# Kernel tuning notes

Measured on AMD Instinct MI355X. Metric: run time of the kernel, lower is better.

## Reference

```python
import jax, jax.numpy as jnp
import numpy as np

NUM_CLASSES = 4
TRAIN_SWITCH = True
TOPO = {1: {0: 1, 1: 0}, 2: {0: 1, 1: 1}, 3: {0: 2, 1: 0}, 4: {0: 1, 1: 0}}


def _sublevel_h0(v, H, W, eight):
    """0-dim sublevel-set persistence of a 2D grid via union-find.

    v: flat numpy array of length H*W. eight: 8-connectivity (gudhi
    T-construction, lower cells = min of cofaces) vs 4-connectivity (dual).
    Returns (pairs, essential_idx): pairs is a list of (birth_idx, death_idx)
    pixel indices with strictly positive persistence; essential_idx is the
    pixel index of the global-min (essential, death = +inf) component.
    """
    N = H * W
    order = np.argsort(v, kind='stable')
    rank = np.empty(N, np.int64)
    rank[order] = np.arange(N)
    parent = np.full(N, -1, np.int64)   # -1 = not yet in filtration
    creator = np.zeros(N, np.int64)     # pixel realizing the component's birth
    pairs = []

    def find(a):
        root = a
        while parent[root] != root:
            root = parent[root]
        while parent[a] != root:
            parent[a], a = root, parent[a]
        return root

    offs = [(-1, 0), (1, 0), (0, -1), (0, 1)]
    if eight:
        offs += [(-1, -1), (-1, 1), (1, -1), (1, 1)]
    for idx in order:
        idx = int(idx)
        r, c = divmod(idx, W)
        parent[idx] = idx
        creator[idx] = idx
        for dr, dc in offs:
            rr, cc = r + dr, c + dc
            if 0 <= rr < H and 0 <= cc < W:
                nb = rr * W + cc
                if parent[nb] >= 0:
                    ra, rb = find(idx), find(nb)
                    if ra != rb:
                        # elder rule: component with earlier (smaller) birth survives
                        if rank[creator[ra]] < rank[creator[rb]]:
                            elder, young = ra, rb
                        else:
                            elder, young = rb, ra
                        if v[idx] > v[creator[young]]:  # drop 0-persistence pairs (gudhi default)
                            pairs.append((int(creator[young]), idx))
                        parent[young] = elder
    ess = int(creator[find(int(order[0]))])
    return pairs, ess


def _diagrams(img):
    """H0 and H1 persistence pairs (as pixel indices) of a 2D image,
    matching gudhi.CubicalComplex(top_dimensional_cells=img).persistence().
    H0: sublevel union-find with 8-connectivity. H1 by Alexander duality:
    superlevel H0 with 4-connectivity, pairs reversed."""
    H, W = img.shape
    v = img.ravel()
    h0, ess = _sublevel_h0(v, H, W, eight=True)
    sup, _ = _sublevel_h0(-v, H, W, eight=False)
    h1 = [(d, b) for (b, d) in sup]  # (saddle birth, max death)
    pers = lambda p: v[p[1]] - v[p[0]]
    h0.sort(key=pers, reverse=True)  # gudhi orders by decreasing persistence
    h1.sort(key=pers, reverse=True)
    return h0, ess, h1


def _dim_loss(flat, pairs, ess_idx, nf):
    """loss_per_dimension: first nf pairs are 'kept' -> (1-pers)^2, missing
    features cost 1 each, extra pairs cost pers^2. Essential (death=inf)
    pair has pers = 1 - birth and sorts first (infinite persistence)."""
    parts = []
    if ess_idx is not None:
        parts.append((1.0 - flat[ess_idx])[None])
    if pairs:
        b = np.asarray([p[0] for p in pairs], np.int64)
        d = np.asarray([p[1] for p in pairs], np.int64)
        parts.append(flat[d] - flat[b])
    pvec = jnp.concatenate(parts) if parts else jnp.zeros((0,), flat.dtype)
    n = pvec.shape[0]
    return jnp.sum((1.0 - pvec[:nf]) ** 2) + float(max(0, nf - n)) + jnp.sum(pvec[nf:] ** 2)


def setup_inputs() -> dict:
    key = jax.random.key(0)
    # (1, batch, classes, H, W); values in [0,1] like softmax probabilities
    x = jax.random.uniform(key, (1, 4, NUM_CLASSES, 64, 64), dtype=jnp.float32)
    return {"x": x}


def reference(x):
    xs = x[0]  # squeeze(0) -> (B, C, H, W)
    if not TRAIN_SWITCH:
        xs = jnp.clip(1.0 - xs, 0.0, 1.0)
    xn = np.asarray(xs)
    B, C, H, W = xn.shape
    loss = jnp.zeros((), jnp.float32)
    for b in range(B):
        for c in range(1, C):  # skip background class 0
            h0, ess, h1 = _diagrams(xn[b, c])
            flat = xs[b, c].ravel()
            loss = loss + _dim_loss(flat, h0, ess, TOPO[c][0])
            loss = loss + _dim_loss(flat, h1, None, TOPO[c][1])
    return loss / B
```

## Files before the change

kernel.cpp:

```cpp
#include <hip/hip_runtime.h>

#define NPIX 4096
#define NT 1024
#define PPT (NPIX / NT)
#define EMPTY 0xFFFFFFFFu
#define FLAGMAGIC 0x00C0FFEEu

__global__ void ph_zero_kernel(float* out) { out[0] = 0.0f; }

__device__ __forceinline__ float kval(unsigned k) {
  unsigned u = (k & 0x80000000u) ? (k & 0x7FFFFFFFu) : ~k;
  return __uint_as_float(u);
}

__global__ __launch_bounds__(NT) void ph_pass_kernel(const float* __restrict__ x,
                                                     float* __restrict__ out,
                                                     unsigned long long* __restrict__ ws64,
                                                     int use_ws) {
  __shared__ unsigned long long pool[2 * NPIX];
  __shared__ unsigned long long claim64[NPIX];
  __shared__ unsigned long long wred[32];
  __shared__ int s_chg[13];
  __shared__ double s_sum[16];
  __shared__ float s_max[16];
  __shared__ int s_cnt[16];

  unsigned long long* sbuf = pool;
  unsigned* hkey = (unsigned*)pool;
  unsigned* hval = hkey + NPIX;
  unsigned* key32 = (unsigned*)(pool + NPIX);
  unsigned short* label = (unsigned short*)(pool + NPIX + NPIX / 2);
  unsigned long long* node = pool + NPIX;

  const int blk = blockIdx.x;
  const int b = blk / 6;
  const int rem = blk % 6;
  const int c = (rem >> 1) + 1;
  const int pass = rem & 1;
  const float* img = x + (size_t)(b * 4 + c) * NPIX;
  const int tid = threadIdx.x;
  const int lane = tid & 63, wid = tid >> 6;
  const int ndirs = pass ? 4 : 8;
  const int drr[8] = {-1, 1, 0, 0, -1, -1, 1, 1};
  const int dcc[8] = { 0, 0,-1, 1, -1,  1, -1, 1};

  if (tid < 13) s_chg[tid] = 0;
  unsigned lmin = EMPTY;
  for (int i = tid; i < NPIX; i += NT) {
    float f = img[i];
    if (pass) f = -f;
    unsigned u = __float_as_uint(f);
    unsigned k = (u & 0x80000000u) ? ~u : (u | 0x80000000u);
    key32[i] = k;
    pool[i] = ~0ull;
    claim64[i] = 0ull;
    lmin = min(lmin, k);
  }
  for (int off = 32; off > 0; off >>= 1)
    lmin = min(lmin, (unsigned)__shfl_xor((int)lmin, off));
  if (lane == 0) wred[wid] = lmin;
  __syncthreads();
  unsigned vmink = (unsigned)wred[0];
  #pragma unroll
  for (int w = 1; w < 16; w++) vmink = min(vmink, (unsigned)wred[w]);

  for (int i = tid; i < NPIX; i += NT) {
    unsigned long long best = ((unsigned long long)key32[i] << 32) | (unsigned)i;
    int bestnb = i;
    int r = i >> 6, cc = i & 63;
    for (int d = 0; d < ndirs; d++) {
      int rr = r + drr[d], c2 = cc + dcc[d];
      if ((unsigned)rr >= 64u || (unsigned)c2 >= 64u) continue;
      int nb = (rr << 6) | c2;
      unsigned long long pn = ((unsigned long long)key32[nb] << 32) | (unsigned)nb;
      if (pn < best) { best = pn; bestnb = nb; }
    }
    label[i] = (unsigned short)bestnb;
  }
  __syncthreads();
  for (int round = 0; round < 6; round++) {
    bool changed = false;
    for (int i = tid; i < NPIX; i += NT) {
      unsigned short l = label[i];
      unsigned short l2 = label[l];
      unsigned short l3 = label[l2];
      unsigned short l4 = label[l3];
      if (l4 != l) { label[i] = l4; changed = true; }
    }
    if (changed) s_chg[round] = 1;
    __syncthreads();
    if (!s_chg[round]) break;
  }

  const int pdr[4] = {1, 0, 1,  1};
  const int pdc[4] = {0, 1, 1, -1};
  const int npd = pass ? 2 : 4;
  for (int i = tid; i < NPIX; i += NT) {
    int r = i >> 6, cc = i & 63;
    unsigned la = label[i];
    unsigned ki = key32[i];
    for (int d = 0; d < npd; d++) {
      int rr = r + pdr[d], c2 = cc + pdc[d];
      if ((unsigned)rr >= 64u || (unsigned)c2 >= 64u) continue;
      int nb = (rr << 6) | c2;
      unsigned lb = label[nb];
      if (lb == la) continue;
      unsigned wkey = max(ki, key32[nb]);
      unsigned pk = la < lb ? ((la << 12) | lb) : ((lb << 12) | la);
      unsigned h = (pk * 2654435761u) >> 20;
      while (true) {
        unsigned old = atomicCAS(&hkey[h], EMPTY, pk);
        if (old == EMPTY || old == pk) { atomicMin(&hval[h], wkey); break; }
        h = (h + 1) & (NPIX - 1);
      }
    }
  }
  __syncthreads();

  unsigned long long item[PPT];
  unsigned mykeys[PPT];
  int cnt = 0;
  #pragma unroll
  for (int q = 0; q < PPT; q++) {
    int s = tid * PPT + q;
    unsigned pk = hkey[s];
    if (pk != EMPTY) item[cnt++] = (((unsigned long long)hval[s]) << 32) | pk;
  }
  #pragma unroll
  for (int t = 0; t < PPT; t++) mykeys[t] = key32[tid + t * NT];
  __syncthreads();
  unsigned inc = (unsigned)cnt;
  for (int off = 1; off < 64; off <<= 1) {
    unsigned v = __shfl_up(inc, off);
    if (lane >= off) inc += v;
  }
  if (lane == 63) wred[wid] = inc;
  __syncthreads();
  if (wid == 0) {
    unsigned wv = (lane < 16) ? (unsigned)wred[lane] : 0u;
    for (int off = 1; off < 16; off <<= 1) {
      unsigned v = __shfl_up(wv, off);
      if (lane >= off) wv += v;
    }
    if (lane < 16) wred[16 + lane] = wv;
  }
  __syncthreads();
  const int M = (int)wred[31];
  const int base0 = (int)((wid ? (unsigned)wred[16 + wid - 1] : 0u) + inc) - cnt;
  for (int q = 0; q < cnt; q++) sbuf[base0 + q] = item[q];
  #pragma unroll
  for (int t = 0; t < PPT; t++) {
    int i = tid + t * NT;
    node[i] = (((unsigned long long)mykeys[t]) << 32) | (unsigned)i;
  }
  if (tid < 2) s_chg[tid] = 0;
  __syncthreads();

  double sumsq = 0.0;
  float maxp = 0.0f;
  int pcnt = 0;
  unsigned ewk[PPT], exa[PPT], exb[PPT];
  unsigned long long erA[PPT], erB[PPT];
  unsigned pmask = 0;
  #pragma unroll
  for (int q = 0; q < PPT; q++) {
    const int j = tid + q * NT;
    if (j < M) {
      const unsigned long long e = sbuf[j];
      ewk[q] = (unsigned)(e >> 32);
      const unsigned pk = (unsigned)(e & 0xFFFFFFu);
      unsigned xa = pk >> 12, xb = pk & 0xFFFu;
      exa[q] = xa; exb[q] = xb;
      erA[q] = node[xa]; erB[q] = node[xb];
      pmask |= 1u << q;
    }
  }
  unsigned long long seqtag = (1ull << 44);
  #pragma unroll
  for (int q = 0; q < PPT; q++) {
    if (pmask & (1u << q)) {
      const int j = tid + q * NT;
      const unsigned long long myval =
          seqtag | (((unsigned long long)(~ewk[q])) << 12) | (unsigned)j;
      unsigned young, elder;
      if (erA[q] < erB[q]) { elder = exa[q]; young = exb[q]; }
      else                 { elder = exb[q]; young = exa[q]; }
      if (claim64[young] < myval) atomicMax(&claim64[young], myval);
      if (claim64[elder] < myval) atomicMax(&claim64[elder], myval);
    }
  }
  int rt = 1;
  while (true) {
    __syncthreads();
    #pragma unroll
    for (int q = 0; q < PPT; q++) {
      if (pmask & (1u << q)) {
        const int j = tid + q * NT;
        const unsigned long long myval =
            seqtag | (((unsigned long long)(~ewk[q])) << 12) | (unsigned)j;
        unsigned young, elder;
        unsigned long long yrec;
        if (erA[q] < erB[q]) { elder = exa[q]; young = exb[q]; yrec = erB[q]; }
        else                 { elder = exb[q]; young = exa[q]; yrec = erA[q]; }
        if (claim64[young] == myval) {
          const unsigned ky = (unsigned)(yrec >> 32);
          if (ewk[q] > ky) {
            float pers = kval(ewk[q]) - kval(ky);
            sumsq += (double)pers * (double)pers;
            maxp = fmaxf(maxp, pers);
            pcnt++;
          }
          node[young] = (yrec & 0xFFFFFFFF00000000ull) | elder;
          pmask &= ~(1u << q);
        }
      }
    }
    if (pmask) s_chg[rt & 1] = 1;
    if (tid == 0) s_chg[(rt + 1) & 1] = 0;
    __syncthreads();
    if (!s_chg[rt & 1]) break;
    rt++; seqtag += (1ull << 44);
    #pragma unroll
    for (int q = 0; q < PPT; q++) {
      if (pmask & (1u << q)) {
        unsigned xa = exa[q], xb = exb[q];
        unsigned long long recA = node[xa], recB = node[xb];
        while ((unsigned)recA != xa) { xa = (unsigned)recA; recA = node[xa]; }
        while ((unsigned)recB != xb) { xb = (unsigned)recB; recB = node[xb]; }
        exa[q] = xa; exb[q] = xb; erA[q] = recA; erB[q] = recB;
        if (xa == xb) {
          pmask &= ~(1u << q);
        } else {
          const int j = tid + q * NT;
          const unsigned long long myval =
              seqtag | (((unsigned long long)(~ewk[q])) << 12) | (unsigned)j;
          unsigned young, elder;
          if (recA < recB) { elder = xa; young = xb; }
          else             { elder = xb; young = xa; }
          if (claim64[young] < myval) atomicMax(&claim64[young], myval);
          if (claim64[elder] < myval) atomicMax(&claim64[elder], myval);
        }
      }
    }
  }
  for (int off = 32; off > 0; off >>= 1) {
    sumsq += __shfl_xor(sumsq, off);
    maxp = fmaxf(maxp, __shfl_xor(maxp, off));
    pcnt += __shfl_xor(pcnt, off);
  }
  if (lane == 0) { s_sum[wid] = sumsq; s_max[wid] = maxp; s_cnt[wid] = pcnt; }
  __syncthreads();

  float contrib = 0.0f;
  if (tid == 0) {
    #pragma unroll
    for (int w = 1; w < 16; w++) {
      sumsq += s_sum[w];
      maxp = fmaxf(maxp, s_max[w]);
      pcnt += s_cnt[w];
    }
    if (pass == 0) {
      const int nf0 = (c == 3) ? 2 : 1;
      float vmin = kval(vmink);
      if (nf0 == 1) {
        contrib = vmin * vmin + (float)sumsq;
      } else if (pcnt >= 1) {
        contrib = vmin * vmin + (1.0f - maxp) * (1.0f - maxp)
                + (float)(sumsq - (double)maxp * (double)maxp);
      } else {
        contrib = vmin * vmin + 1.0f;
      }
    } else {
      const int nf1 = (c == 2) ? 1 : 0;
      if (nf1 == 0) contrib = (float)sumsq;
      else contrib = (pcnt >= 1)
        ? ((1.0f - maxp) * (1.0f - maxp) + (float)(sumsq - (double)maxp * (double)maxp))
        : 1.0f;
    }
    contrib *= 0.25f;
    if (use_ws) {
      atomicExch(&ws64[blk],
                 (((unsigned long long)__float_as_uint(contrib)) << 32) | FLAGMAGIC);
    } else {
      atomicAdd(out, contrib);
    }
  }
  if (use_ws && blk == 0 && wid == 0) {
    float v = 0.0f;
    if (lane < 24) {
      while (true) {
        unsigned long long r = atomicAdd(&ws64[lane], 0ull);
        if ((unsigned)r == FLAGMAGIC) { v = __uint_as_float((unsigned)(r >> 32)); break; }
      }
    }
    for (int off = 32; off > 0; off >>= 1) v += __shfl_xor(v, off);
    if (lane == 0) out[0] = v;
  }
}

extern "C" void kernel_launch(void* const* d_in, const int* in_sizes, int n_in,
                              void* d_out, int out_size, void* d_ws, size_t ws_size,
                              hipStream_t stream) {
  const float* x = (const float*)d_in[0];
  float* out = (float*)d_out;
  if (ws_size >= 24 * sizeof(unsigned long long)) {
    ph_pass_kernel<<<24, NT, 0, stream>>>(x, out, (unsigned long long*)d_ws, 1);
  } else {
    ph_zero_kernel<<<1, 1, 0, stream>>>(out);
    ph_pass_kernel<<<24, NT, 0, stream>>>(x, out, nullptr, 0);
  }
}
```

Baseline: 94.32 us.

## Hand off the union-find merge tail to a single wavefront when few edges remain

The iterative claim/resolve merge rounds now count the remaining active edges with a ballot-based block reduction. When at most 160 remain, the edges are compacted into a shared queue and one wavefront finishes the rounds alone, with no block-wide barriers. This targets the many cheap tail rounds where full 1024-thread __syncthreads dominate. It relies on wavefront-level lockstep visibility of LDS writes and a compiler fence, and an iteration guard could silently truncate work.

```diff
diff --git a/kernel.cpp b/kernel.cpp
--- a/kernel.cpp
+++ b/kernel.cpp
@@ -5,12 +5,18 @@
 #define PPT (NPIX / NT)
 #define EMPTY 0xFFFFFFFFu
 #define FLAGMAGIC 0x00C0FFEEu
+#define TAKEOVER 160
 
 __global__ void ph_zero_kernel(float* out) { out[0] = 0.0f; }
 
 __device__ __forceinline__ float kval(unsigned k) {
   unsigned u = (k & 0x80000000u) ? (k & 0x7FFFFFFFu) : ~k;
   return __uint_as_float(u);
+}
+
+__device__ __forceinline__ void memfence_compiler() {
+  __asm__ volatile("" ::: "memory");
+  __builtin_amdgcn_sched_barrier(0);
 }
 
 __global__ __launch_bounds__(NT) void ph_pass_kernel(const float* __restrict__ x,
@@ -21,6 +27,7 @@
   __shared__ unsigned long long claim64[NPIX];
   __shared__ unsigned long long wred[32];
   __shared__ int s_chg[13];
+  __shared__ int s_qn;
   __shared__ double s_sum[16];
   __shared__ float s_max[16];
   __shared__ int s_cnt[16];
@@ -31,6 +38,8 @@
   unsigned* key32 = (unsigned*)(pool + NPIX);
   unsigned short* label = (unsigned short*)(pool + NPIX + NPIX / 2);
   unsigned long long* node = pool + NPIX;
+  unsigned long long* q1 = pool;
+  unsigned* q2 = (unsigned*)(pool + TAKEOVER);
 
   const int blk = blockIdx.x;
   const int b = blk / 6;
@@ -45,6 +54,7 @@
   const int dcc[8] = { 0, 0,-1, 1, -1,  1, -1, 1};
 
   if (tid < 13) s_chg[tid] = 0;
+  if (tid == 0) s_qn = 0;
   unsigned lmin = EMPTY;
   for (int i = tid; i < NPIX; i += NT) {
     float f = img[i];
@@ -153,7 +163,6 @@
     int i = tid + t * NT;
     node[i] = (((unsigned long long)mykeys[t]) << 32) | (unsigned)i;
   }
-  if (tid < 2) s_chg[tid] = 0;
   __syncthreads();
 
   double sumsq = 0.0;
@@ -189,7 +198,6 @@
       if (claim64[elder] < myval) atomicMax(&claim64[elder], myval);
     }
   }
-  int rt = 1;
   while (true) {
     __syncthreads();
     #pragma unroll
@@ -215,11 +223,89 @@
         }
       }
     }
-    if (pmask) s_chg[rt & 1] = 1;
-    if (tid == 0) s_chg[(rt + 1) & 1] = 0;
+    unsigned pc = 0;
+    #pragma unroll
+    for (int q = 0; q < PPT; q++)
+      pc += (unsigned)__popcll(__ballot((pmask >> q) & 1));
+    if (lane == 0) wred[wid] = pc;
     __syncthreads();
-    if (!s_chg[rt & 1]) break;
-    rt++; seqtag += (1ull << 44);
+    unsigned tot = 0;
+    #pragma unroll
+    for (int w = 0; w < 16; w++) tot += (unsigned)wred[w];
+    if (tot == 0) break;
+    if (tot <= TAKEOVER) {
+      #pragma unroll
+      for (int q = 0; q < PPT; q++) {
+        if (pmask & (1u << q)) {
+          int slot = atomicAdd(&s_qn, 1);
+          q1[slot] = (((unsigned long long)ewk[q]) << 32) | (unsigned)(tid + q * NT);
+          q2[slot] = (exa[q] << 12) | exb[q];
+        }
+      }
+      __syncthreads();
+      if (wid == 0) {
+        const int n = s_qn;
+        unsigned qwk[3], qid[3], qxa[3], qxb[3];
+        unsigned long long qrA[3], qrB[3];
+        unsigned qp = 0;
+        for (int s = lane, sl = 0; s < n && sl < 3; s += 64, sl++) {
+          qwk[sl] = (unsigned)(q1[s] >> 32);
+          qid[sl] = (unsigned)(q1[s] & 0xFFFu);
+          qxa[sl] = q2[s] >> 12; qxb[sl] = q2[s] & 0xFFFu;
+          qp |= 1u << sl;
+        }
+        int guard = 0;
+        while (__ballot(qp)) {
+          if (++guard > 4096) break;
+          seqtag += (1ull << 44);
+          #pragma unroll
+          for (int s = 0; s < 3; s++) {
+            if (qp & (1u << s)) {
+              unsigned xa = qxa[s], xb = qxb[s];
+              unsigned long long recA = node[xa], recB = node[xb];
+              while ((unsigned)recA != xa) { xa = (unsigned)recA; recA = node[xa]; }
+              while ((unsigned)recB != xb) { xb = (unsigned)recB; recB = node[xb]; }
+              qxa[s] = xa; qxb[s] = xb; qrA[s] = recA; qrB[s] = recB;
+              if (xa == xb) { qp &= ~(1u << s); continue; }
+              const unsigned long long myval =
+                  seqtag | (((unsigned long long)(~qwk[s])) << 12) | qid[s];
+              unsigned young, elder;
+              if (recA < recB) { elder = xa; young = xb; }
+              else             { elder = xb; young = xa; }
+              if (claim64[young] < myval) atomicMax(&claim64[young], myval);
+              if (claim64[elder] < myval) atomicMax(&claim64[elder], myval);
+            }
+          }
+          memfence_compiler();
+          #pragma unroll
+          for (int s = 0; s < 3; s++) {
+            if (qp & (1u << s)) {
+              const unsigned long long myval =
+                  seqtag | (((unsigned long long)(~qwk[s])) << 12) | qid[s];
+              unsigned young, elder;
+              unsigned long long yrec;
+              if (qrA[s] < qrB[s]) { elder = qxa[s]; young = qxb[s]; yrec = qrB[s]; }
+              else                 { elder = qxb[s]; young = qxa[s]; yrec = qrA[s]; }
+              if (claim64[young] == myval) {
+                const unsigned ky = (unsigned)(yrec >> 32);
+                if (qwk[s] > ky) {
+                  float pers = kval(qwk[s]) - kval(ky);
+                  sumsq += (double)pers * (double)pers;
+                  maxp = fmaxf(maxp, pers);
+                  pcnt++;
+                }
+                node[young] = (yrec & 0xFFFFFFFF00000000ull) | elder;
+                qp &= ~(1u << s);
+              }
+            }
+          }
+          memfence_compiler();
+        }
+      }
+      __syncthreads();
+      break;
+    }
+    seqtag += (1ull << 44);
     #pragma unroll
     for (int q = 0; q < PPT; q++) {
       if (pmask & (1u << q)) {
```

Result: slower. 96.65 us (+2.5%).

## Give each thread four contiguous pixels with vectorized loads and register-held labels

Applied to the files above, without the earlier changes.

Changes the pixel-to-thread mapping from strided to four contiguous pixels per thread. Global reads and shared-memory inits, key/label/node stores use float4/uint4/ushort4 vector accesses. Neighbor keys are gathered once and reused for the initial min-neighbor labeling and the edge emission, which is unrolled with explicit neighbor cases. Labels stay in registers across pointer-jumping rounds. The goal is fewer shared-memory transactions and less index arithmetic in the early phases, at the cost of more registers and more bank conflicts from the contiguous mapping.

```diff
diff --git a/kernel.cpp b/kernel.cpp
--- a/kernel.cpp
+++ b/kernel.cpp
@@ -2,7 +2,7 @@
 
 #define NPIX 4096
 #define NT 1024
-#define PPT (NPIX / NT)
+#define PPT 4
 #define EMPTY 0xFFFFFFFFu
 #define FLAGMAGIC 0x00C0FFEEu
 
@@ -17,8 +17,8 @@
                                                      float* __restrict__ out,
                                                      unsigned long long* __restrict__ ws64,
                                                      int use_ws) {
-  __shared__ unsigned long long pool[2 * NPIX];
-  __shared__ unsigned long long claim64[NPIX];
+  __shared__ __align__(16) unsigned long long pool[2 * NPIX];
+  __shared__ __align__(16) unsigned long long claim64[NPIX];
   __shared__ unsigned long long wred[32];
   __shared__ int s_chg[13];
   __shared__ double s_sum[16];
@@ -40,22 +40,33 @@
   const float* img = x + (size_t)(b * 4 + c) * NPIX;
   const int tid = threadIdx.x;
   const int lane = tid & 63, wid = tid >> 6;
-  const int ndirs = pass ? 4 : 8;
-  const int drr[8] = {-1, 1, 0, 0, -1, -1, 1, 1};
-  const int dcc[8] = { 0, 0,-1, 1, -1,  1, -1, 1};
+
+  const int i0 = tid << 2;
+  const bool hasL = (tid & 15) != 0;
+  const bool hasR = (tid & 15) != 15;
+  const bool hasU = tid >= 16;
+  const bool hasD = tid < 1008;
 
   if (tid < 13) s_chg[tid] = 0;
-  unsigned lmin = EMPTY;
-  for (int i = tid; i < NPIX; i += NT) {
-    float f = img[i];
-    if (pass) f = -f;
-    unsigned u = __float_as_uint(f);
-    unsigned k = (u & 0x80000000u) ? ~u : (u | 0x80000000u);
-    key32[i] = k;
-    pool[i] = ~0ull;
-    claim64[i] = 0ull;
-    lmin = min(lmin, k);
-  }
+  unsigned k[4];
+  {
+    float4 v = ((const float4*)img)[tid];
+    if (pass) { v.x = -v.x; v.y = -v.y; v.z = -v.z; v.w = -v.w; }
+    unsigned u;
+    u = __float_as_uint(v.x); k[0] = (u & 0x80000000u) ? ~u : (u | 0x80000000u);
+    u = __float_as_uint(v.y); k[1] = (u & 0x80000000u) ? ~u : (u | 0x80000000u);
+    u = __float_as_uint(v.z); k[2] = (u & 0x80000000u) ? ~u : (u | 0x80000000u);
+    u = __float_as_uint(v.w); k[3] = (u & 0x80000000u) ? ~u : (u | 0x80000000u);
+    uint4 t; t.x = k[0]; t.y = k[1]; t.z = k[2]; t.w = k[3];
+    ((uint4*)key32)[tid] = t;
+    ulonglong2 e; e.x = ~0ull; e.y = ~0ull;
+    ((ulonglong2*)pool)[2 * tid] = e;
+    ((ulonglong2*)pool)[2 * tid + 1] = e;
+    ulonglong2 z; z.x = 0ull; z.y = 0ull;
+    ((ulonglong2*)claim64)[2 * tid] = z;
+    ((ulonglong2*)claim64)[2 * tid + 1] = z;
+  }
+  unsigned lmin = min(min(k[0], k[1]), min(k[2], k[3]));
   for (int off = 32; off > 0; off >>= 1)
     lmin = min(lmin, (unsigned)__shfl_xor((int)lmin, off));
   if (lane == 0) wred[wid] = lmin;
@@ -64,70 +75,118 @@
   #pragma unroll
   for (int w = 1; w < 16; w++) vmink = min(vmink, (unsigned)wred[w]);
 
-  for (int i = tid; i < NPIX; i += NT) {
-    unsigned long long best = ((unsigned long long)key32[i] << 32) | (unsigned)i;
-    int bestnb = i;
-    int r = i >> 6, cc = i & 63;
-    for (int d = 0; d < ndirs; d++) {
-      int rr = r + drr[d], c2 = cc + dcc[d];
-      if ((unsigned)rr >= 64u || (unsigned)c2 >= 64u) continue;
-      int nb = (rr << 6) | c2;
-      unsigned long long pn = ((unsigned long long)key32[nb] << 32) | (unsigned)nb;
-      if (pn < best) { best = pn; bestnb = nb; }
-    }
-    label[i] = (unsigned short)bestnb;
+  unsigned ku[4], kd[4];
+  unsigned kl = EMPTY, kr = EMPTY, kul = EMPTY, kur = EMPTY, kdl = EMPTY, kdr = EMPTY;
+  if (hasU) { uint4 t = ((const uint4*)key32)[tid - 16]; ku[0]=t.x; ku[1]=t.y; ku[2]=t.z; ku[3]=t.w; }
+  else { ku[0]=ku[1]=ku[2]=ku[3]=EMPTY; }
+  if (hasD) { uint4 t = ((const uint4*)key32)[tid + 16]; kd[0]=t.x; kd[1]=t.y; kd[2]=t.z; kd[3]=t.w; }
+  else { kd[0]=kd[1]=kd[2]=kd[3]=EMPTY; }
+  if (hasL) kl = key32[i0 - 1];
+  if (hasR) kr = key32[i0 + 4];
+  if (!pass) {
+    if (hasU && hasL) kul = key32[i0 - 65];
+    if (hasU && hasR) kur = key32[i0 - 60];
+    if (hasD && hasL) kdl = key32[i0 + 63];
+    if (hasD && hasR) kdr = key32[i0 + 68];
+  }
+  unsigned short cur[4];
+  #pragma unroll
+  for (int q = 0; q < 4; q++) {
+    const int i = i0 + q;
+    unsigned long long best = ((unsigned long long)k[q] << 32) | (unsigned)i;
+    auto upd = [&](bool v, unsigned kn, int nb) {
+      if (v) {
+        unsigned long long pn = ((unsigned long long)kn << 32) | (unsigned)nb;
+        if (pn < best) best = pn;
+      }
+    };
+    upd(hasU, ku[q], i - 64);
+    upd(hasD, kd[q], i + 64);
+    upd(q > 0 ? true : hasL, q > 0 ? k[q - 1] : kl, i - 1);
+    upd(q < 3 ? true : hasR, q < 3 ? k[q + 1] : kr, i + 1);
+    if (!pass) {
+      upd(hasU && (q > 0 ? true : hasL), q > 0 ? ku[q - 1] : kul, i - 65);
+      upd(hasU && (q < 3 ? true : hasR), q < 3 ? ku[q + 1] : kur, i - 63);
+      upd(hasD && (q > 0 ? true : hasL), q > 0 ? kd[q - 1] : kdl, i + 63);
+      upd(hasD && (q < 3 ? true : hasR), q < 3 ? kd[q + 1] : kdr, i + 65);
+    }
+    cur[q] = (unsigned short)(unsigned)best;
+  }
+  {
+    ushort4 t; t.x = cur[0]; t.y = cur[1]; t.z = cur[2]; t.w = cur[3];
+    ((ushort4*)label)[tid] = t;
   }
   __syncthreads();
   for (int round = 0; round < 6; round++) {
     bool changed = false;
-    for (int i = tid; i < NPIX; i += NT) {
-      unsigned short l = label[i];
+    #pragma unroll
+    for (int q = 0; q < 4; q++) {
+      unsigned short l = cur[q];
       unsigned short l2 = label[l];
       unsigned short l3 = label[l2];
       unsigned short l4 = label[l3];
-      if (l4 != l) { label[i] = l4; changed = true; }
-    }
+      if (l4 != l) changed = true;
+      cur[q] = l4;
+    }
+    ushort4 t; t.x = cur[0]; t.y = cur[1]; t.z = cur[2]; t.w = cur[3];
+    ((ushort4*)label)[tid] = t;
     if (changed) s_chg[round] = 1;
     __syncthreads();
     if (!s_chg[round]) break;
   }
 
-  const int pdr[4] = {1, 0, 1,  1};
-  const int pdc[4] = {0, 1, 1, -1};
-  const int npd = pass ? 2 : 4;
-  for (int i = tid; i < NPIX; i += NT) {
-    int r = i >> 6, cc = i & 63;
-    unsigned la = label[i];
-    unsigned ki = key32[i];
-    for (int d = 0; d < npd; d++) {
-      int rr = r + pdr[d], c2 = cc + pdc[d];
-      if ((unsigned)rr >= 64u || (unsigned)c2 >= 64u) continue;
-      int nb = (rr << 6) | c2;
-      unsigned lb = label[nb];
-      if (lb == la) continue;
-      unsigned wkey = max(ki, key32[nb]);
-      unsigned pk = la < lb ? ((la << 12) | lb) : ((lb << 12) | la);
-      unsigned h = (pk * 2654435761u) >> 20;
-      while (true) {
-        unsigned old = atomicCAS(&hkey[h], EMPTY, pk);
-        if (old == EMPTY || old == pk) { atomicMin(&hval[h], wkey); break; }
-        h = (h + 1) & (NPIX - 1);
-      }
-    }
-  }
-  __syncthreads();
-
-  unsigned long long item[PPT];
-  unsigned mykeys[PPT];
+  auto emit = [&](unsigned la, unsigned lb, unsigned ka_, unsigned kb_) {
+    if (la == lb) return;
+    unsigned wkey = max(ka_, kb_);
+    unsigned pk = la < lb ? ((la << 12) | lb) : ((lb << 12) | la);
+    unsigned h = (pk * 2654435761u) >> 20;
+    while (true) {
+      unsigned old = atomicCAS(&hkey[h], EMPTY, pk);
+      if (old == EMPTY || old == pk) { atomicMin(&hval[h], wkey); break; }
+      h = (h + 1) & (NPIX - 1);
+    }
+  };
+  {
+    unsigned short lr16 = 0, ld[4] = {0, 0, 0, 0}, ldl16 = 0, ldr16 = 0;
+    if (hasR) lr16 = label[i0 + 4];
+    if (hasD) { ushort4 t = ((const ushort4*)label)[tid + 16]; ld[0]=t.x; ld[1]=t.y; ld[2]=t.z; ld[3]=t.w; }
+    if (!pass && hasD) {
+      if (hasL) ldl16 = label[i0 + 63];
+      if (hasR) ldr16 = label[i0 + 68];
+    }
+    emit(cur[0], cur[1], k[0], k[1]);
+    emit(cur[1], cur[2], k[1], k[2]);
+    emit(cur[2], cur[3], k[2], k[3]);
+    if (hasR) emit(cur[3], lr16, k[3], kr);
+    if (hasD) {
+      emit(cur[0], ld[0], k[0], kd[0]);
+      emit(cur[1], ld[1], k[1], kd[1]);
+      emit(cur[2], ld[2], k[2], kd[2]);
+      emit(cur[3], ld[3], k[3], kd[3]);
+      if (!pass) {
+        emit(cur[0], ld[1], k[0], kd[1]);
+        emit(cur[1], ld[2], k[1], kd[2]);
+        emit(cur[2], ld[3], k[2], kd[3]);
+        if (hasR) emit(cur[3], ldr16, k[3], kdr);
+        emit(cur[1], ld[0], k[1], kd[0]);
+        emit(cur[2], ld[1], k[2], kd[1]);
+        emit(cur[3], ld[2], k[3], kd[2]);
+        if (hasL) emit(cur[0], ldl16, k[0], kdl);
+      }
+    }
+  }
+  __syncthreads();
+
+  unsigned long long item[4];
   int cnt = 0;
-  #pragma unroll
-  for (int q = 0; q < PPT; q++) {
-    int s = tid * PPT + q;
-    unsigned pk = hkey[s];
-    if (pk != EMPTY) item[cnt++] = (((unsigned long long)hval[s]) << 32) | pk;
-  }
-  #pragma unroll
-  for (int t = 0; t < PPT; t++) mykeys[t] = key32[tid + t * NT];
+  {
+    uint4 hk = ((const uint4*)hkey)[tid];
+    uint4 hv = ((const uint4*)hval)[tid];
+    if (hk.x != EMPTY) item[cnt++] = (((unsigned long long)hv.x) << 32) | hk.x;
+    if (hk.y != EMPTY) item[cnt++] = (((unsigned long long)hv.y) << 32) | hk.y;
+    if (hk.z != EMPTY) item[cnt++] = (((unsigned long long)hv.z) << 32) | hk.z;
+    if (hk.w != EMPTY) item[cnt++] = (((unsigned long long)hv.w) << 32) | hk.w;
+  }
   __syncthreads();
   unsigned inc = (unsigned)cnt;
   for (int off = 1; off < 64; off <<= 1) {
@@ -148,10 +207,14 @@
   const int M = (int)wred[31];
   const int base0 = (int)((wid ? (unsigned)wred[16 + wid - 1] : 0u) + inc) - cnt;
   for (int q = 0; q < cnt; q++) sbuf[base0 + q] = item[q];
-  #pragma unroll
-  for (int t = 0; t < PPT; t++) {
-    int i = tid + t * NT;
-    node[i] = (((unsigned long long)mykeys[t]) << 32) | (unsigned)i;
+  {
+    ulonglong2 n0, n1;
+    n0.x = (((unsigned long long)k[0]) << 32) | (unsigned)i0;
+    n0.y = (((unsigned long long)k[1]) << 32) | (unsigned)(i0 + 1);
+    n1.x = (((unsigned long long)k[2]) << 32) | (unsigned)(i0 + 2);
+    n1.y = (((unsigned long long)k[3]) << 32) | (unsigned)(i0 + 3);
+    ((ulonglong2*)node)[2 * tid] = n0;
+    ((ulonglong2*)node)[2 * tid + 1] = n1;
   }
   if (tid < 2) s_chg[tid] = 0;
   __syncthreads();
```

New measurement: 89.96 us. 1.05x faster.
